# Optimization experiments

Measured on AMD Instinct MI355X. Metric: run time of the kernel, lower is better.

Reference implementation:

```python
import jax, jax.numpy as jnp
import numpy as np

NUM_LAYERS = 3
HIDDEN = 128
N_NODES = 50000
N_EDGES = 600000


def setup_inputs() -> dict:
    key = jax.random.key(0)
    ks = jax.random.split(key, 5)
    x = jax.random.normal(ks[0], (N_NODES, HIDDEN), dtype=jnp.float32)
    edge_index = jax.random.randint(ks[1], (2, N_EDGES), 0, N_NODES, dtype=jnp.int32)
    scale = 1.0 / np.sqrt(HIDDEN)
    # SAGEConv params per layer: lin_l (neighbor path, with bias), lin_r (root path, no bias)
    Wl = jax.random.uniform(ks[2], (NUM_LAYERS, HIDDEN, HIDDEN), jnp.float32, -scale, scale)
    bl = jnp.zeros((NUM_LAYERS, HIDDEN), dtype=jnp.float32)
    Wr = jax.random.uniform(ks[3], (NUM_LAYERS, HIDDEN, HIDDEN), jnp.float32, -scale, scale)
    return {"x": x, "edge_index": edge_index, "Wl": Wl, "bl": bl, "Wr": Wr}


def reference(x, edge_index, Wl, bl, Wr):
    # PyG SAGEConv (aggr='mean', root_weight=True):
    #   out = lin_l(mean_{j in N(i)} x_j) + lin_r(x_i)
    src = edge_index[0]
    dst = edge_index[1]
    n = x.shape[0]
    deg = jax.ops.segment_sum(jnp.ones(src.shape[0], dtype=x.dtype), dst, num_segments=n)
    inv_deg = (1.0 / jnp.maximum(deg, 1.0))[:, None]  # [N,1]
    h = x
    for i in range(NUM_LAYERS):
        agg = jax.ops.segment_sum(h[src], dst, num_segments=n) * inv_deg  # [N,H]
        h = agg @ Wl[i].T + bl[i] + h @ Wr[i].T
        if i < NUM_LAYERS - 1:
            h = jax.nn.relu(h)  # dropout_rate=0 -> Identity
    return h
```

## Files before the change

kernel.cpp:

```cpp
#include <hip/hip_runtime.h>
#include <hip/hip_bf16.h>

#define H 128

using bf16x8 = __attribute__((ext_vector_type(8))) short;
using f32x4  = __attribute__((ext_vector_type(4))) float;

__device__ inline unsigned short f2bf(float f) {
    unsigned u = __float_as_uint(f);
    unsigned r = (u + 0x7fffu + ((u >> 16) & 1u)) >> 16;
    return (unsigned short)r;
}
__device__ inline float bf2f(unsigned short b) {
    return __uint_as_float(((unsigned)b) << 16);
}


__global__ void k_zero_i32(int* __restrict__ p, int n) {
    int i = blockIdx.x * blockDim.x + threadIdx.x;
    if (i < n) p[i] = 0;
}

__global__ void k_count(const int* __restrict__ dst, int* __restrict__ deg, int e) {
    int i = blockIdx.x * blockDim.x + threadIdx.x;
    if (i < e) atomicAdd(&deg[dst[i]], 1);
}

__global__ __launch_bounds__(1024) void k_scan_partial(const int* __restrict__ deg,
                                                       int* __restrict__ partials, int n) {
    __shared__ int sm[1024];
    int t = threadIdx.x;
    int i = blockIdx.x * 1024 + t;
    sm[t] = (i < n) ? deg[i] : 0;
    __syncthreads();
    for (int s = 512; s > 0; s >>= 1) {
        if (t < s) sm[t] += sm[t + s];
        __syncthreads();
    }
    if (t == 0) partials[blockIdx.x] = sm[0];
}

__global__ __launch_bounds__(64) void k_scan_base(int* __restrict__ partials, int nb,
                                                  int* __restrict__ offsets, int n) {
    __shared__ int sm[64];
    int t = threadIdx.x;
    int v = (t < nb) ? partials[t] : 0;
    sm[t] = v;
    __syncthreads();
    for (int off = 1; off < 64; off <<= 1) {
        int x = 0;
        if (t >= off) x = sm[t - off];
        __syncthreads();
        if (t >= off) sm[t] += x;
        __syncthreads();
    }
    if (t < nb) partials[t] = sm[t] - v;
    if (t == 63) offsets[n] = sm[63];
}

__global__ __launch_bounds__(1024) void k_scan_final(const int* __restrict__ deg,
                                                     const int* __restrict__ partials,
                                                     int* __restrict__ offsets,
                                                     int* __restrict__ cursor,
                                                     float* __restrict__ inv_deg, int n) {
    __shared__ int sm[1024];
    int t = threadIdx.x;
    int b = blockIdx.x;
    int i = b * 1024 + t;
    int v = (i < n) ? deg[i] : 0;
    sm[t] = v;
    __syncthreads();
    for (int off = 1; off < 1024; off <<= 1) {
        int x = 0;
        if (t >= off) x = sm[t - off];
        __syncthreads();
        if (t >= off) sm[t] += x;
        __syncthreads();
    }
    if (i < n) {
        int excl = partials[b] + sm[t] - v;
        offsets[i] = excl;
        cursor[i]  = excl;
        inv_deg[i] = 1.0f / fmaxf((float)v, 1.0f);
    }
}

__global__ void k_fill(const int* __restrict__ src, const int* __restrict__ dst,
                       int* __restrict__ cursor, int* __restrict__ csr, int e) {
    int i = blockIdx.x * blockDim.x + threadIdx.x;
    if (i < e) {
        int d = dst[i];
        int pos = atomicAdd(&cursor[d], 1);
        csr[pos] = src[i];
    }
}

__global__ void k_wsplit(const float* __restrict__ Wl, const float* __restrict__ Wr,
                         unsigned short* __restrict__ Wf, int total) {
    int idx = blockIdx.x * blockDim.x + threadIdx.x;
    if (idx >= total) return;
    int l = idx >> 12;
    int rem = idx & 4095;
    int s = rem >> 9;
    int c = (rem >> 6) & 7;
    int lane = rem & 63;
    int j = c * 16 + (lane & 15);
    int k0 = s * 32 + (lane >> 4) * 8;
    size_t fc = (size_t)(idx >> 6);
    size_t hbase = (fc * 2 * 64 + lane) * 8;
    size_t lbase = hbase + 512;
    for (int jj = 0; jj < 8; ++jj) {
        int k = k0 + jj;
        float v;
        if (k < H) v = Wl[(size_t)l * H * H + j * H + k];
        else       v = Wr[(size_t)l * H * H + j * H + (k - H)];
        unsigned short hi = f2bf(v);
        unsigned short lo = f2bf(v - bf2f(hi));
        Wf[hbase + jj] = hi;
        Wf[lbase + jj] = lo;
    }
}

__global__ __launch_bounds__(256) void k_fused(const float* __restrict__ h,
                                               const int* __restrict__ csr,
                                               const int* __restrict__ offsets,
                                               const float* __restrict__ inv_deg,
                                               const unsigned short* __restrict__ Wf,
                                               const float* __restrict__ bias,
                                               float* __restrict__ out, int n, int relu) {
    __shared__ unsigned short AL[4096];

    int t = threadIdx.x;

    {
        int grp = t >> 5;
        int l4 = t & 31;
        const float4* hv = (const float4*)h;
#pragma unroll
        for (int i = 0; i < 2; ++i) {
            int bn = grp * 2 + i;
            int gnode = blockIdx.x * 16 + bn;
            if (gnode >= n) break;
            int ps = offsets[gnode];
            int pe = offsets[gnode + 1];
            float4 a0 = make_float4(0.f, 0.f, 0.f, 0.f);
            float4 a1 = make_float4(0.f, 0.f, 0.f, 0.f);
            float4 a2 = make_float4(0.f, 0.f, 0.f, 0.f);
            float4 a3 = make_float4(0.f, 0.f, 0.f, 0.f);
            int p = ps;
            for (; p + 3 < pe; p += 4) {
                int i0 = csr[p], i1 = csr[p + 1], i2 = csr[p + 2], i3 = csr[p + 3];
                float4 v0 = hv[(size_t)i0 * 32 + l4];
                float4 v1 = hv[(size_t)i1 * 32 + l4];
                float4 v2 = hv[(size_t)i2 * 32 + l4];
                float4 v3 = hv[(size_t)i3 * 32 + l4];
                a0.x += v0.x; a0.y += v0.y; a0.z += v0.z; a0.w += v0.w;
                a1.x += v1.x; a1.y += v1.y; a1.z += v1.z; a1.w += v1.w;
                a2.x += v2.x; a2.y += v2.y; a2.z += v2.z; a2.w += v2.w;
                a3.x += v3.x; a3.y += v3.y; a3.z += v3.z; a3.w += v3.w;
            }
            for (; p < pe; ++p) {
                int i0 = csr[p];
                float4 v0 = hv[(size_t)i0 * 32 + l4];
                a0.x += v0.x; a0.y += v0.y; a0.z += v0.z; a0.w += v0.w;
            }
            float w = inv_deg[gnode];
            float4 acc;
            acc.x = ((a0.x + a1.x) + (a2.x + a3.x)) * w;
            acc.y = ((a0.y + a1.y) + (a2.y + a3.y)) * w;
            acc.z = ((a0.z + a1.z) + (a2.z + a3.z)) * w;
            acc.w = ((a0.w + a1.w) + (a2.w + a3.w)) * w;

            int r16 = bn;
            int s = l4 >> 3;
            int kq = (l4 >> 1) & 3;
            int e0 = (l4 & 1) * 4;
            int offh = ((s * 2 + 0) * 64 + kq * 16 + r16) * 8 + e0;
            int offl = offh + 512;

            ushort4 hi4, lo4;
            hi4.x = f2bf(acc.x); lo4.x = f2bf(acc.x - bf2f(hi4.x));
            hi4.y = f2bf(acc.y); lo4.y = f2bf(acc.y - bf2f(hi4.y));
            hi4.z = f2bf(acc.z); lo4.z = f2bf(acc.z - bf2f(hi4.z));
            hi4.w = f2bf(acc.w); lo4.w = f2bf(acc.w - bf2f(hi4.w));
            *(ushort4*)(&AL[offh]) = hi4;
            *(ushort4*)(&AL[offl]) = lo4;
        }
    }
    __syncthreads();

    int wv = t >> 6;
    int lane = t & 63;
    int r16 = lane & 15;
    int kq = lane >> 4;

    f32x4 acc[2];
    acc[0] = (f32x4){0.f, 0.f, 0.f, 0.f};
    acc[1] = (f32x4){0.f, 0.f, 0.f, 0.f};

#pragma unroll
    for (int s = 0; s < 4; ++s) {
        int ab = ((s * 2) * 64 + lane) * 8;
        bf16x8 ah = *(const bf16x8*)(&AL[ab]);
        bf16x8 al = *(const bf16x8*)(&AL[ab + 512]);
#pragma unroll
        for (int j = 0; j < 2; ++j) {
            int c = wv * 2 + j;
            size_t wb = (((size_t)(s * 8 + c) * 2) * 64 + lane) * 8;
            bf16x8 b_hi = *(const bf16x8*)(Wf + wb);
            bf16x8 b_lo = *(const bf16x8*)(Wf + wb + 512);
            acc[j] = __builtin_amdgcn_mfma_f32_16x16x32_bf16(ah, b_hi, acc[j], 0, 0, 0);
            acc[j] = __builtin_amdgcn_mfma_f32_16x16x32_bf16(ah, b_lo, acc[j], 0, 0, 0);
            acc[j] = __builtin_amdgcn_mfma_f32_16x16x32_bf16(al, b_hi, acc[j], 0, 0, 0);
        }
    }

    int grow = blockIdx.x * 16 + r16;
    bool rok = grow < n;
#pragma unroll
    for (int s = 4; s < 8; ++s) {
        bf16x8 ah = {}, al = {};
        if (rok) {
            const float* hp = h + (size_t)grow * H + (s - 4) * 32 + kq * 8;
            float4 v0 = *(const float4*)hp;
            float4 v1 = *(const float4*)(hp + 4);
            unsigned short x;
            x = f2bf(v0.x); ah[0] = (short)x; al[0] = (short)f2bf(v0.x - bf2f(x));
            x = f2bf(v0.y); ah[1] = (short)x; al[1] = (short)f2bf(v0.y - bf2f(x));
            x = f2bf(v0.z); ah[2] = (short)x; al[2] = (short)f2bf(v0.z - bf2f(x));
            x = f2bf(v0.w); ah[3] = (short)x; al[3] = (short)f2bf(v0.w - bf2f(x));
            x = f2bf(v1.x); ah[4] = (short)x; al[4] = (short)f2bf(v1.x - bf2f(x));
            x = f2bf(v1.y); ah[5] = (short)x; al[5] = (short)f2bf(v1.y - bf2f(x));
            x = f2bf(v1.z); ah[6] = (short)x; al[6] = (short)f2bf(v1.z - bf2f(x));
            x = f2bf(v1.w); ah[7] = (short)x; al[7] = (short)f2bf(v1.w - bf2f(x));
        }
#pragma unroll
        for (int j = 0; j < 2; ++j) {
            int c = wv * 2 + j;
            size_t wb = (((size_t)(s * 8 + c) * 2) * 64 + lane) * 8;
            bf16x8 b_hi = *(const bf16x8*)(Wf + wb);
            bf16x8 b_lo = *(const bf16x8*)(Wf + wb + 512);
            acc[j] = __builtin_amdgcn_mfma_f32_16x16x32_bf16(ah, b_hi, acc[j], 0, 0, 0);
            acc[j] = __builtin_amdgcn_mfma_f32_16x16x32_bf16(ah, b_lo, acc[j], 0, 0, 0);
            acc[j] = __builtin_amdgcn_mfma_f32_16x16x32_bf16(al, b_hi, acc[j], 0, 0, 0);
        }
    }

#pragma unroll
    for (int j = 0; j < 2; ++j) {
        int col = (wv * 2 + j) * 16 + r16;
        float b = bias[col];
#pragma unroll
        for (int r = 0; r < 4; ++r) {
            int go = blockIdx.x * 16 + kq * 4 + r;
            if (go < n) {
                float v = acc[j][r] + b;
                if (relu) v = fmaxf(v, 0.f);
                out[(size_t)go * H + col] = v;
            }
        }
    }
}


extern "C" void kernel_launch(void* const* d_in, const int* in_sizes, int n_in,
                              void* d_out, int out_size, void* d_ws, size_t ws_size,
                              hipStream_t stream) {
    const float* x  = (const float*)d_in[0];
    const int*   ei = (const int*)d_in[1];
    const float* Wl = (const float*)d_in[2];
    const float* bl = (const float*)d_in[3];
    const float* Wr = (const float*)d_in[4];
    float* out = (float*)d_out;

    int n = in_sizes[0] / H;
    int e = in_sizes[1] / 2;
    const int* srcp = ei;
    const int* dstp = ei + e;

    char* w = (char*)d_ws;
    auto alloc = [&](size_t bytes) {
        char* p = w;
        w += (bytes + 255) & ~(size_t)255;
        return p;
    };
    int nb = (n + 1023) / 1024;
    int*            csr      = (int*)alloc((size_t)e * 4);
    int*            offsets  = (int*)alloc((size_t)(n + 1) * 4);
    int*            cursor   = (int*)alloc((size_t)n * 4);
    int*            deg      = (int*)alloc((size_t)n * 4);
    float*          inv_deg  = (float*)alloc((size_t)n * 4);
    int*            partials = (int*)alloc(64 * 4);
    unsigned short* Wf       = (unsigned short*)alloc((size_t)3 * 8 * 8 * 2 * 64 * 8 * 2);
    float*          hbuf     = (float*)alloc((size_t)n * H * 4);

    k_zero_i32<<<(n + 255) / 256, 256, 0, stream>>>(deg, n);
    k_count<<<(e + 255) / 256, 256, 0, stream>>>(dstp, deg, e);
    k_scan_partial<<<nb, 1024, 0, stream>>>(deg, partials, n);
    k_scan_base<<<1, 64, 0, stream>>>(partials, nb, offsets, n);
    k_scan_final<<<nb, 1024, 0, stream>>>(deg, partials, offsets, cursor, inv_deg, n);
    k_fill<<<(e + 255) / 256, 256, 0, stream>>>(srcp, dstp, cursor, csr, e);
    int wtot = 3 * 8 * 8 * 64;
    k_wsplit<<<(wtot + 255) / 256, 256, 0, stream>>>(Wl, Wr, Wf, wtot);

    const float* hin[3]  = {x, out, hbuf};
    float*       hout[3] = {out, hbuf, out};
    int nblk = (n + 15) / 16;
    for (int l = 0; l < 3; ++l) {
        k_fused<<<nblk, 256, 0, stream>>>(hin[l], csr, offsets, inv_deg,
                                          Wf + (size_t)l * 8 * 8 * 2 * 64 * 8,
                                          bl + (size_t)l * H, hout[l], n, l < 2 ? 1 : 0);
    }
}
```

Before: 352.7 us.

## Interleave gather loops of two nodes and swizzle LDS A-tile layout

The aggregation phase now processes both nodes assigned to a 32-lane group together, issuing eight independent neighbour-row loads per iteration instead of four, to raise memory-level parallelism and hide gather latency. Each node uses two accumulators instead of four. The LDS layout for the hi/lo bf16 A tile changes to a row-major form with an XOR swizzle to cut bank conflicts on writes, and the MFMA read indexing is updated to match. The cost is more registers and tail loops that run serially when degrees differ.

```diff
diff --git a/kernel.cpp b/kernel.cpp
--- a/kernel.cpp
+++ b/kernel.cpp
@@ -14,6 +14,8 @@
 __device__ inline float bf2f(unsigned short b) {
     return __uint_as_float(((unsigned)b) << 16);
 }
+
+#define ADD4(d, v) { d.x += v.x; d.y += v.y; d.z += v.z; d.w += v.w; }
 
 
 __global__ void k_zero_i32(int* __restrict__ p, int n) {
@@ -136,55 +138,84 @@
         int grp = t >> 5;
         int l4 = t & 31;
         const float4* hv = (const float4*)h;
-#pragma unroll
-        for (int i = 0; i < 2; ++i) {
-            int bn = grp * 2 + i;
-            int gnode = blockIdx.x * 16 + bn;
-            if (gnode >= n) break;
-            int ps = offsets[gnode];
-            int pe = offsets[gnode + 1];
-            float4 a0 = make_float4(0.f, 0.f, 0.f, 0.f);
-            float4 a1 = make_float4(0.f, 0.f, 0.f, 0.f);
-            float4 a2 = make_float4(0.f, 0.f, 0.f, 0.f);
-            float4 a3 = make_float4(0.f, 0.f, 0.f, 0.f);
-            int p = ps;
-            for (; p + 3 < pe; p += 4) {
-                int i0 = csr[p], i1 = csr[p + 1], i2 = csr[p + 2], i3 = csr[p + 3];
-                float4 v0 = hv[(size_t)i0 * 32 + l4];
-                float4 v1 = hv[(size_t)i1 * 32 + l4];
-                float4 v2 = hv[(size_t)i2 * 32 + l4];
-                float4 v3 = hv[(size_t)i3 * 32 + l4];
-                a0.x += v0.x; a0.y += v0.y; a0.z += v0.z; a0.w += v0.w;
-                a1.x += v1.x; a1.y += v1.y; a1.z += v1.z; a1.w += v1.w;
-                a2.x += v2.x; a2.y += v2.y; a2.z += v2.z; a2.w += v2.w;
-                a3.x += v3.x; a3.y += v3.y; a3.z += v3.z; a3.w += v3.w;
-            }
-            for (; p < pe; ++p) {
-                int i0 = csr[p];
-                float4 v0 = hv[(size_t)i0 * 32 + l4];
-                a0.x += v0.x; a0.y += v0.y; a0.z += v0.z; a0.w += v0.w;
-            }
-            float w = inv_deg[gnode];
+        int bn0 = grp * 2, bn1 = bn0 + 1;
+        int g0 = blockIdx.x * 16 + bn0;
+        int g1 = g0 + 1;
+        float4 A0 = make_float4(0.f, 0.f, 0.f, 0.f), A1 = A0;
+        float4 B0 = A0, B1 = A0;
+        int p0 = 0, q0 = 0, p1 = 0, q1 = 0;
+        if (g0 < n) { p0 = offsets[g0]; q0 = offsets[g0 + 1]; }
+        if (g1 < n) { p1 = offsets[g1]; q1 = offsets[g1 + 1]; }
+
+        while (p0 + 3 < q0 && p1 + 3 < q1) {
+            int iA0 = csr[p0], iA1 = csr[p0 + 1], iA2 = csr[p0 + 2], iA3 = csr[p0 + 3];
+            int iB0 = csr[p1], iB1 = csr[p1 + 1], iB2 = csr[p1 + 2], iB3 = csr[p1 + 3];
+            float4 vA0 = hv[(size_t)iA0 * 32 + l4];
+            float4 vA1 = hv[(size_t)iA1 * 32 + l4];
+            float4 vA2 = hv[(size_t)iA2 * 32 + l4];
+            float4 vA3 = hv[(size_t)iA3 * 32 + l4];
+            float4 vB0 = hv[(size_t)iB0 * 32 + l4];
+            float4 vB1 = hv[(size_t)iB1 * 32 + l4];
+            float4 vB2 = hv[(size_t)iB2 * 32 + l4];
+            float4 vB3 = hv[(size_t)iB3 * 32 + l4];
+            ADD4(A0, vA0); ADD4(A1, vA1); ADD4(A0, vA2); ADD4(A1, vA3);
+            ADD4(B0, vB0); ADD4(B1, vB1); ADD4(B0, vB2); ADD4(B1, vB3);
+            p0 += 4; p1 += 4;
+        }
+        for (; p0 + 3 < q0; p0 += 4) {
+            int i0 = csr[p0], i1 = csr[p0 + 1], i2 = csr[p0 + 2], i3 = csr[p0 + 3];
+            float4 v0 = hv[(size_t)i0 * 32 + l4];
+            float4 v1 = hv[(size_t)i1 * 32 + l4];
+            float4 v2 = hv[(size_t)i2 * 32 + l4];
+            float4 v3 = hv[(size_t)i3 * 32 + l4];
+            ADD4(A0, v0); ADD4(A1, v1); ADD4(A0, v2); ADD4(A1, v3);
+        }
+        for (; p0 < q0; ++p0) {
+            int i0 = csr[p0];
+            float4 v0 = hv[(size_t)i0 * 32 + l4];
+            ADD4(A0, v0);
+        }
+        for (; p1 + 3 < q1; p1 += 4) {
+            int i0 = csr[p1], i1 = csr[p1 + 1], i2 = csr[p1 + 2], i3 = csr[p1 + 3];
+            float4 v0 = hv[(size_t)i0 * 32 + l4];
+            float4 v1 = hv[(size_t)i1 * 32 + l4];
+            float4 v2 = hv[(size_t)i2 * 32 + l4];
+            float4 v3 = hv[(size_t)i3 * 32 + l4];
+            ADD4(B0, v0); ADD4(B1, v1); ADD4(B0, v2); ADD4(B1, v3);
+        }
+        for (; p1 < q1; ++p1) {
+            int i0 = csr[p1];
+            float4 v0 = hv[(size_t)i0 * 32 + l4];
+            ADD4(B0, v0);
+        }
+
+        if (g0 < n) {
+            float w = inv_deg[g0];
             float4 acc;
-            acc.x = ((a0.x + a1.x) + (a2.x + a3.x)) * w;
-            acc.y = ((a0.y + a1.y) + (a2.y + a3.y)) * w;
-            acc.z = ((a0.z + a1.z) + (a2.z + a3.z)) * w;
-            acc.w = ((a0.w + a1.w) + (a2.w + a3.w)) * w;
-
-            int r16 = bn;
-            int s = l4 >> 3;
-            int kq = (l4 >> 1) & 3;
-            int e0 = (l4 & 1) * 4;
-            int offh = ((s * 2 + 0) * 64 + kq * 16 + r16) * 8 + e0;
-            int offl = offh + 512;
-
+            acc.x = (A0.x + A1.x) * w; acc.y = (A0.y + A1.y) * w;
+            acc.z = (A0.z + A1.z) * w; acc.w = (A0.w + A1.w) * w;
+            int wb = (bn0 * 256 + l4 * 4) ^ ((bn0 & 7) << 3);
             ushort4 hi4, lo4;
             hi4.x = f2bf(acc.x); lo4.x = f2bf(acc.x - bf2f(hi4.x));
             hi4.y = f2bf(acc.y); lo4.y = f2bf(acc.y - bf2f(hi4.y));
             hi4.z = f2bf(acc.z); lo4.z = f2bf(acc.z - bf2f(hi4.z));
             hi4.w = f2bf(acc.w); lo4.w = f2bf(acc.w - bf2f(hi4.w));
-            *(ushort4*)(&AL[offh]) = hi4;
-            *(ushort4*)(&AL[offl]) = lo4;
+            *(ushort4*)(&AL[wb])       = hi4;
+            *(ushort4*)(&AL[wb + 128]) = lo4;
+        }
+        if (g1 < n) {
+            float w = inv_deg[g1];
+            float4 acc;
+            acc.x = (B0.x + B1.x) * w; acc.y = (B0.y + B1.y) * w;
+            acc.z = (B0.z + B1.z) * w; acc.w = (B0.w + B1.w) * w;
+            int wb = (bn1 * 256 + l4 * 4) ^ ((bn1 & 7) << 3);
+            ushort4 hi4, lo4;
+            hi4.x = f2bf(acc.x); lo4.x = f2bf(acc.x - bf2f(hi4.x));
+            hi4.y = f2bf(acc.y); lo4.y = f2bf(acc.y - bf2f(hi4.y));
+            hi4.z = f2bf(acc.z); lo4.z = f2bf(acc.z - bf2f(hi4.z));
+            hi4.w = f2bf(acc.w); lo4.w = f2bf(acc.w - bf2f(hi4.w));
+            *(ushort4*)(&AL[wb])       = hi4;
+            *(ushort4*)(&AL[wb + 128]) = lo4;
         }
     }
     __syncthreads();
@@ -200,9 +231,9 @@
 
 #pragma unroll
     for (int s = 0; s < 4; ++s) {
-        int ab = ((s * 2) * 64 + lane) * 8;
-        bf16x8 ah = *(const bf16x8*)(&AL[ab]);
-        bf16x8 al = *(const bf16x8*)(&AL[ab + 512]);
+        int rb = (r16 * 256 + s * 32 + kq * 8) ^ ((r16 & 7) << 3);
+        bf16x8 ah = *(const bf16x8*)(&AL[rb]);
+        bf16x8 al = *(const bf16x8*)(&AL[rb + 128]);
 #pragma unroll
         for (int j = 0; j < 2; ++j) {
             int c = wv * 2 + j;
```

Result: slower. 370.2 us (+5.0%).

## Use 512-thread blocks: one node per 32-lane group and one column tile per wave

Applied to the files above, without the earlier changes.

The fused SAGE layer kernel now launches 512 threads per 16-node block. Each 32-thread group gathers one node's neighbours instead of two in sequence, and each of 8 waves computes one 16-column output tile instead of two. The LDS layout for the aggregated rows becomes row-major with an XOR swizzle to avoid bank conflicts. This doubles gather parallelism to hide irregular memory latency, but reduces per-wave MFMA work and may lower occupancy.

```diff
diff --git a/kernel.cpp b/kernel.cpp
--- a/kernel.cpp
+++ b/kernel.cpp
@@ -14,6 +14,8 @@
 __device__ inline float bf2f(unsigned short b) {
     return __uint_as_float(((unsigned)b) << 16);
 }
+
+#define ADD4(d, v) { d.x += v.x; d.y += v.y; d.z += v.z; d.w += v.w; }
 
 
 __global__ void k_zero_i32(int* __restrict__ p, int n) {
@@ -121,7 +123,7 @@
     }
 }
 
-__global__ __launch_bounds__(256) void k_fused(const float* __restrict__ h,
+__global__ __launch_bounds__(512) void k_fused(const float* __restrict__ h,
                                                const int* __restrict__ csr,
                                                const int* __restrict__ offsets,
                                                const float* __restrict__ inv_deg,
@@ -133,20 +135,15 @@
     int t = threadIdx.x;
 
     {
-        int grp = t >> 5;
+        int bn = t >> 5;
         int l4 = t & 31;
         const float4* hv = (const float4*)h;
-#pragma unroll
-        for (int i = 0; i < 2; ++i) {
-            int bn = grp * 2 + i;
-            int gnode = blockIdx.x * 16 + bn;
-            if (gnode >= n) break;
+        int gnode = blockIdx.x * 16 + bn;
+        if (gnode < n) {
             int ps = offsets[gnode];
             int pe = offsets[gnode + 1];
             float4 a0 = make_float4(0.f, 0.f, 0.f, 0.f);
-            float4 a1 = make_float4(0.f, 0.f, 0.f, 0.f);
-            float4 a2 = make_float4(0.f, 0.f, 0.f, 0.f);
-            float4 a3 = make_float4(0.f, 0.f, 0.f, 0.f);
+            float4 a1 = a0, a2 = a0, a3 = a0;
             int p = ps;
             for (; p + 3 < pe; p += 4) {
                 int i0 = csr[p], i1 = csr[p + 1], i2 = csr[p + 2], i3 = csr[p + 3];
@@ -154,15 +151,12 @@
                 float4 v1 = hv[(size_t)i1 * 32 + l4];
                 float4 v2 = hv[(size_t)i2 * 32 + l4];
                 float4 v3 = hv[(size_t)i3 * 32 + l4];
-                a0.x += v0.x; a0.y += v0.y; a0.z += v0.z; a0.w += v0.w;
-                a1.x += v1.x; a1.y += v1.y; a1.z += v1.z; a1.w += v1.w;
-                a2.x += v2.x; a2.y += v2.y; a2.z += v2.z; a2.w += v2.w;
-                a3.x += v3.x; a3.y += v3.y; a3.z += v3.z; a3.w += v3.w;
+                ADD4(a0, v0); ADD4(a1, v1); ADD4(a2, v2); ADD4(a3, v3);
             }
             for (; p < pe; ++p) {
                 int i0 = csr[p];
                 float4 v0 = hv[(size_t)i0 * 32 + l4];
-                a0.x += v0.x; a0.y += v0.y; a0.z += v0.z; a0.w += v0.w;
+                ADD4(a0, v0);
             }
             float w = inv_deg[gnode];
             float4 acc;
@@ -171,20 +165,14 @@
             acc.z = ((a0.z + a1.z) + (a2.z + a3.z)) * w;
             acc.w = ((a0.w + a1.w) + (a2.w + a3.w)) * w;
 
-            int r16 = bn;
-            int s = l4 >> 3;
-            int kq = (l4 >> 1) & 3;
-            int e0 = (l4 & 1) * 4;
-            int offh = ((s * 2 + 0) * 64 + kq * 16 + r16) * 8 + e0;
-            int offl = offh + 512;
-
+            int wb = (bn * 256 + l4 * 4) ^ ((bn & 7) << 3);
             ushort4 hi4, lo4;
             hi4.x = f2bf(acc.x); lo4.x = f2bf(acc.x - bf2f(hi4.x));
             hi4.y = f2bf(acc.y); lo4.y = f2bf(acc.y - bf2f(hi4.y));
             hi4.z = f2bf(acc.z); lo4.z = f2bf(acc.z - bf2f(hi4.z));
             hi4.w = f2bf(acc.w); lo4.w = f2bf(acc.w - bf2f(hi4.w));
-            *(ushort4*)(&AL[offh]) = hi4;
-            *(ushort4*)(&AL[offl]) = lo4;
+            *(ushort4*)(&AL[wb])       = hi4;
+            *(ushort4*)(&AL[wb + 128]) = lo4;
         }
     }
     __syncthreads();
@@ -194,25 +182,19 @@
     int r16 = lane & 15;
     int kq = lane >> 4;
 
-    f32x4 acc[2];
-    acc[0] = (f32x4){0.f, 0.f, 0.f, 0.f};
-    acc[1] = (f32x4){0.f, 0.f, 0.f, 0.f};
+    f32x4 acc = (f32x4){0.f, 0.f, 0.f, 0.f};
 
 #pragma unroll
     for (int s = 0; s < 4; ++s) {
-        int ab = ((s * 2) * 64 + lane) * 8;
-        bf16x8 ah = *(const bf16x8*)(&AL[ab]);
-        bf16x8 al = *(const bf16x8*)(&AL[ab + 512]);
-#pragma unroll
-        for (int j = 0; j < 2; ++j) {
-            int c = wv * 2 + j;
-            size_t wb = (((size_t)(s * 8 + c) * 2) * 64 + lane) * 8;
-            bf16x8 b_hi = *(const bf16x8*)(Wf + wb);
-            bf16x8 b_lo = *(const bf16x8*)(Wf + wb + 512);
-            acc[j] = __builtin_amdgcn_mfma_f32_16x16x32_bf16(ah, b_hi, acc[j], 0, 0, 0);
-            acc[j] = __builtin_amdgcn_mfma_f32_16x16x32_bf16(ah, b_lo, acc[j], 0, 0, 0);
-            acc[j] = __builtin_amdgcn_mfma_f32_16x16x32_bf16(al, b_hi, acc[j], 0, 0, 0);
-        }
+        int rb = (r16 * 256 + s * 32 + kq * 8) ^ ((r16 & 7) << 3);
+        bf16x8 ah = *(const bf16x8*)(&AL[rb]);
+        bf16x8 al = *(const bf16x8*)(&AL[rb + 128]);
+        size_t wb = (((size_t)(s * 8 + wv) * 2) * 64 + lane) * 8;
+        bf16x8 b_hi = *(const bf16x8*)(Wf + wb);
+        bf16x8 b_lo = *(const bf16x8*)(Wf + wb + 512);
+        acc = __builtin_amdgcn_mfma_f32_16x16x32_bf16(ah, b_hi, acc, 0, 0, 0);
+        acc = __builtin_amdgcn_mfma_f32_16x16x32_bf16(ah, b_lo, acc, 0, 0, 0);
+        acc = __builtin_amdgcn_mfma_f32_16x16x32_bf16(al, b_hi, acc, 0, 0, 0);
     }
 
     int grow = blockIdx.x * 16 + r16;
@@ -234,27 +216,22 @@
             x = f2bf(v1.z); ah[6] = (short)x; al[6] = (short)f2bf(v1.z - bf2f(x));
             x = f2bf(v1.w); ah[7] = (short)x; al[7] = (short)f2bf(v1.w - bf2f(x));
         }
-#pragma unroll
-        for (int j = 0; j < 2; ++j) {
-            int c = wv * 2 + j;
-            size_t wb = (((size_t)(s * 8 + c) * 2) * 64 + lane) * 8;
-            bf16x8 b_hi = *(const bf16x8*)(Wf + wb);
-            bf16x8 b_lo = *(const bf16x8*)(Wf + wb + 512);
-            acc[j] = __builtin_amdgcn_mfma_f32_16x16x32_bf16(ah, b_hi, acc[j], 0, 0, 0);
-            acc[j] = __builtin_amdgcn_mfma_f32_16x16x32_bf16(ah, b_lo, acc[j], 0, 0, 0);
-            acc[j] = __builtin_amdgcn_mfma_f32_16x16x32_bf16(al, b_hi, acc[j], 0, 0, 0);
-        }
-    }
-
-#pragma unroll
-    for (int j = 0; j < 2; ++j) {
-        int col = (wv * 2 + j) * 16 + r16;
+        size_t wb = (((size_t)(s * 8 + wv) * 2) * 64 + lane) * 8;
+        bf16x8 b_hi = *(const bf16x8*)(Wf + wb);
+        bf16x8 b_lo = *(const bf16x8*)(Wf + wb + 512);
+        acc = __builtin_amdgcn_mfma_f32_16x16x32_bf16(ah, b_hi, acc, 0, 0, 0);
+        acc = __builtin_amdgcn_mfma_f32_16x16x32_bf16(ah, b_lo, acc, 0, 0, 0);
+        acc = __builtin_amdgcn_mfma_f32_16x16x32_bf16(al, b_hi, acc, 0, 0, 0);
+    }
+
+    {
+        int col = wv * 16 + r16;
         float b = bias[col];
 #pragma unroll
         for (int r = 0; r < 4; ++r) {
             int go = blockIdx.x * 16 + kq * 4 + r;
             if (go < n) {
-                float v = acc[j][r] + b;
+                float v = acc[r] + b;
                 if (relu) v = fmaxf(v, 0.f);
                 out[(size_t)go * H + col] = v;
             }
@@ -307,7 +284,7 @@
     float*       hout[3] = {out, hbuf, out};
     int nblk = (n + 15) / 16;
     for (int l = 0; l < 3; ++l) {
-        k_fused<<<nblk, 256, 0, stream>>>(hin[l], csr, offsets, inv_deg,
+        k_fused<<<nblk, 512, 0, stream>>>(hin[l], csr, offsets, inv_deg,
                                           Wf + (size_t)l * 8 * 8 * 2 * 64 * 8,
                                           bl + (size_t)l * H, hout[l], n, l < 2 ? 1 : 0);
     }
```

Result: slower. 379.6 us (+7.6%).
